# Kernel optimization log

Hardware: AMD Instinct MI355X
Metric: run time of the kernel (lower is better)

The kernel has to match this reference:

```python
import jax, jax.numpy as jnp
import numpy as np

B, N = 8192, 64  # batch of small SPD matrices (SPDnet covariance descriptors)
EPS = 1e-3


def setup_inputs() -> dict:
    key = jax.random.key(0)
    A = jax.random.normal(key, (B, N, N), dtype=jnp.float32)
    # Make strictly SPD: X = A A^T / N + eps*I
    X = jnp.matmul(A, jnp.swapaxes(A, -1, -2)) / N + EPS * jnp.eye(N, dtype=jnp.float32)
    return {"X": X}


def reference(X):
    # LogEig: eigendecompose each SPD matrix, take log of eigenvalues, reconstruct.
    # eigh returns ascending eigenvalues w (b, n) and orthonormal eigenvectors v (b, n, n)
    w, v = jnp.linalg.eigh(X)
    # Y = V diag(log w) V^T
    Y = jnp.einsum('bik,bk,bjk->bij', v, jnp.log(w), v)
    return Y
```

## Files before the change

### kernel.cpp

```cpp
#include <hip/hip_runtime.h>
#include <math.h>

#define NN 4096
#define MAX_SWEEPS 12

typedef float f2 __attribute__((ext_vector_type(2)));

constexpr int psi_step(int k) { return ((k << 1) & 63) ^ ((k & 32) ? 3 : 0); }
struct CycTab {
  int c[63];
  constexpr CycTab() : c{} {
    int x = 1;
    for (int j = 0; j < 63; ++j) { c[j] = x; x = psi_step(x); }
  }
};
static constexpr CycTab CYC{};

__device__ __forceinline__ float bperm(int addr, float x) {
  return __int_as_float(__builtin_amdgcn_ds_bpermute(addr, __float_as_int(x)));
}
__device__ __forceinline__ void wave_lds_fence() {
  asm volatile("s_waitcnt lgkmcnt(0)" ::: "memory");
}

__device__ __forceinline__ f2 colrot(f2 cs, f2 xy) {
  f2 t, d;
  asm("v_pk_mul_f32 %0, %1, %2 op_sel:[1,1] op_sel_hi:[0,1] neg_lo:[1,0]"
      : "=v"(t) : "v"(cs), "v"(xy));
  asm("v_pk_fma_f32 %0, %1, %2, %3 op_sel:[0,0,0] op_sel_hi:[1,0,1]"
      : "=v"(d) : "v"(cs), "v"(xy), "v"(t));
  return d;
}
__device__ __forceinline__ f2 rowrot(f2 cs, f2 a, f2 p) {
  f2 t, d;
  asm("v_pk_mul_f32 %0, %1, %2 op_sel:[1,1] op_sel_hi:[1,0] neg_lo:[1,0] neg_hi:[1,0]"
      : "=v"(t) : "v"(cs), "v"(p));
  asm("v_pk_fma_f32 %0, %1, %2, %3 op_sel:[0,0,0] op_sel_hi:[0,1,1]"
      : "=v"(d) : "v"(cs), "v"(a), "v"(t));
  return d;
}

__global__ __launch_bounds__(256, 2) void logeig_jacobi_pk4(
    const float* __restrict__ X, float* __restrict__ out) {
  __shared__ float SH[4][1024];
  __shared__ f2 ANG[4][64];
  const int tid = threadIdx.x;
  const int lane = tid & 63;
  const int wid = tid >> 6;
  const size_t base = ((size_t)blockIdx.x * 4 + wid) * NN;
  float* lds = SH[wid];
  f2* ang = ANG[wid];

  f2 a2[32], v2[32];

  {
    const float4* Xg = (const float4*)(X + base);
    float4* L4 = (float4*)lds;
    for (int ch = 0; ch < 4; ++ch) {
#pragma unroll
      for (int i = 0; i < 4; ++i) L4[lane + 64 * i] = Xg[ch * 256 + lane + 64 * i];
      wave_lds_fence();
      if ((lane >> 4) == ch) {
        const int lr = (lane & 15) << 6;
#pragma unroll
        for (int r = 0; r < 64; ++r) {
          const float val = lds[lr + (lane ^ r)];
          if (r & 1) a2[r >> 1].y = val; else a2[r >> 1].x = val;
        }
      }
      wave_lds_fence();
    }
  }
#pragma unroll
  for (int t = 1; t < 32; ++t) { v2[t].x = 0.0f; v2[t].y = 0.0f; }
  v2[0].x = 1.0f; v2[0].y = 0.0f;

  int m = 1, B0 = 2, B1 = 4, B2 = 8, B3 = 16, B4 = 32;

#pragma unroll 1
  for (int sw = 0; sw < MAX_SWEEPS; ++sw) {
#pragma unroll 1
    for (int rr = 0; rr < 63; ++rr) {
      const int maddr = (lane ^ m) << 2;
      const float mydg = a2[0].x;
      const float otdg = bperm(maddr, mydg);
      const float apq = 0.5f * (a2[0].y + bperm(maddr, a2[0].y));
      const bool isq = (lane ^ m) < lane;
      const float app = isq ? otdg : mydg;
      const float aqq = isq ? mydg : otdg;
      float c = 1.0f, s = 0.0f;
      if (fabsf(apq) > 1e-37f) {
        const float tau = (aqq - app) / (2.0f * apq);
        float tt = 1.0f / (fabsf(tau) + sqrtf(1.0f + tau * tau));
        tt = (tau >= 0.0f) ? tt : -tt;
        c = rsqrtf(1.0f + tt * tt);
        s = tt * c;
      }
      const float st = isq ? -s : s;
      const f2 cst0 = {c, st};
      ang[lane] = cst0;
      wave_lds_fence();

      {
        const int Bv[5] = {B0, B1, B2, B3, B4};
        int ui = lane;
#pragma unroll
        for (int t = 0; t < 32; ++t) {
          const int slot = t ^ (t >> 1);
          const f2 csg = (t == 0) ? cst0 : ang[ui];
          a2[slot] = colrot(csg, a2[slot]);
          v2[slot] = colrot(csg, v2[slot]);
          if (t < 31) ui ^= Bv[__builtin_ctz(t + 1)];
        }
      }

#pragma unroll
      for (int t = 0; t < 32; ++t) {
        f2 p;
        p.x = bperm(maddr, a2[t].x);
        p.y = bperm(maddr, a2[t].y);
        a2[t] = rowrot(cst0, a2[t], p);
      }

      {
        const int h = CYC.c[0];
        const float ta = (h & 1) ? a2[h >> 1].y : a2[h >> 1].x;
        const float tv = (h & 1) ? v2[h >> 1].y : v2[h >> 1].x;
#pragma unroll
        for (int j = 0; j < 62; ++j) {
          const int dd = CYC.c[j], ss2 = CYC.c[j + 1];
          const float sa = (ss2 & 1) ? a2[ss2 >> 1].y : a2[ss2 >> 1].x;
          const float sv = (ss2 & 1) ? v2[ss2 >> 1].y : v2[ss2 >> 1].x;
          if (dd & 1) { a2[dd >> 1].y = sa; v2[dd >> 1].y = sv; }
          else        { a2[dd >> 1].x = sa; v2[dd >> 1].x = sv; }
        }
        const int l_ = CYC.c[62];
        if (l_ & 1) { a2[l_ >> 1].y = ta; v2[l_ >> 1].y = tv; }
        else        { a2[l_ >> 1].x = ta; v2[l_ >> 1].x = tv; }
      }

      const int nB4 = m ^ B0;
      m = B0; B0 = B1; B1 = B2; B2 = B3; B3 = B4; B4 = nB4;
    }

    float offs = a2[0].y * a2[0].y, dias = a2[0].x * a2[0].x;
#pragma unroll
    for (int t = 1; t < 32; ++t) {
      offs = fmaf(a2[t].x, a2[t].x, offs);
      offs = fmaf(a2[t].y, a2[t].y, offs);
    }
#pragma unroll
    for (int o = 1; o < 64; o <<= 1) {
      offs += __shfl_xor(offs, o);
      dias += __shfl_xor(dias, o);
    }
    if (offs <= 1e-13f * dias) break;
  }

  const float ll = logf(fmaxf(a2[0].x, 1e-30f));
#pragma unroll
  for (int r = 0; r < 64; ++r) {
    const float lr_ = __shfl_xor(ll, r);
    if (r & 1) a2[r >> 1].y = lr_; else a2[r >> 1].x = lr_;
  }
  float* Og = out + base;
  for (int tt = 0; tt < 4; ++tt) {
    if ((lane >> 4) == tt) {
      const int lr = (lane & 15) << 6;
#pragma unroll
      for (int t = 0; t < 32; ++t) {
        const f2 w = v2[t] * a2[t];
        lds[lr + ((2 * t) ^ lane)] = w.x;
        lds[lr + ((2 * t + 1) ^ lane)] = w.y;
      }
    }
    wave_lds_fence();
#pragma unroll 1
    for (int ii = 0; ii < 16; ++ii) {
      const float* Wrow = lds + (ii << 6);
      float acc0 = 0.0f, acc1 = 0.0f;
#pragma unroll
      for (int t = 0; t < 32; ++t) {
        acc0 = fmaf(Wrow[lane ^ (2 * t)], v2[t].x, acc0);
        acc1 = fmaf(Wrow[lane ^ (2 * t + 1)], v2[t].y, acc1);
      }
      Og[((tt << 4) + ii) * 64 + lane] = acc0 + acc1;
    }
    wave_lds_fence();
  }
}

extern "C" void kernel_launch(void* const* d_in, const int* in_sizes, int n_in,
                              void* d_out, int out_size, void* d_ws, size_t ws_size,
                              hipStream_t stream) {
  const float* X = (const float*)d_in[0];
  float* out = (float*)d_out;
  const int nmat = in_sizes[0] / NN;
  logeig_jacobi_pk4<<<nmat / 4, 256, 0, stream>>>(X, out);
}
```

Measured before the change: 5.862 ms.

## Fuse column and row rotations, prefetch next pivot values via bpermute

Fuses the column-rotation and row-rotation loops into one pass. Each slot's partner-lane values are fetched with bpermute before the local column rotation, and the partner's column rotation is recomputed locally with a sign-adjusted variant. It also prefetches the next round's diagonal and off-diagonal partner values early in the loop, taking them off the critical path of the angle computation, and replaces the divisions with hardware reciprocals. This removes one full pass over the registers and overlaps LDS permute latency with arithmetic, at the cost of extra rotation FLOPs and reduced precision in the angle computation.

```diff
diff --git a/kernel.cpp b/kernel.cpp
--- a/kernel.cpp
+++ b/kernel.cpp
@@ -22,12 +22,23 @@
 __device__ __forceinline__ void wave_lds_fence() {
   asm volatile("s_waitcnt lgkmcnt(0)" ::: "memory");
 }
+__device__ __forceinline__ float fast_rcp(float x) {
+  float r; asm("v_rcp_f32 %0, %1" : "=v"(r) : "v"(x)); return r;
+}
 
 __device__ __forceinline__ f2 colrot(f2 cs, f2 xy) {
   f2 t, d;
   asm("v_pk_mul_f32 %0, %1, %2 op_sel:[1,1] op_sel_hi:[0,1] neg_lo:[1,0]"
       : "=v"(t) : "v"(cs), "v"(xy));
   asm("v_pk_fma_f32 %0, %1, %2, %3 op_sel:[0,0,0] op_sel_hi:[1,0,1]"
+      : "=v"(d) : "v"(cs), "v"(xy), "v"(t));
+  return d;
+}
+__device__ __forceinline__ f2 colrotP(f2 cs, f2 xy) {
+  f2 t, d;
+  asm("v_pk_mul_f32 %0, %1, %2 op_sel:[1,1] op_sel_hi:[0,1]"
+      : "=v"(t) : "v"(cs), "v"(xy));
+  asm("v_pk_fma_f32 %0, %1, %2, %3 op_sel:[0,0,0] op_sel_hi:[1,0,1] neg_hi:[1,0,0]"
       : "=v"(d) : "v"(cs), "v"(xy), "v"(t));
   return d;
 }
@@ -77,23 +88,26 @@
 
   int m = 1, B0 = 2, B1 = 4, B2 = 8, B3 = 16, B4 = 32;
 
+  float otdg_pf = bperm((lane ^ 1) << 2, a2[0].x);
+  float sym_pf  = bperm((lane ^ 1) << 2, a2[0].y);
+
 #pragma unroll 1
   for (int sw = 0; sw < MAX_SWEEPS; ++sw) {
 #pragma unroll 1
     for (int rr = 0; rr < 63; ++rr) {
       const int maddr = (lane ^ m) << 2;
       const float mydg = a2[0].x;
-      const float otdg = bperm(maddr, mydg);
-      const float apq = 0.5f * (a2[0].y + bperm(maddr, a2[0].y));
+      const float apq = 0.5f * (a2[0].y + sym_pf);
       const bool isq = (lane ^ m) < lane;
-      const float app = isq ? otdg : mydg;
-      const float aqq = isq ? mydg : otdg;
+      const float app = isq ? otdg_pf : mydg;
+      const float aqq = isq ? mydg : otdg_pf;
       float c = 1.0f, s = 0.0f;
       if (fabsf(apq) > 1e-37f) {
-        const float tau = (aqq - app) / (2.0f * apq);
-        float tt = 1.0f / (fabsf(tau) + sqrtf(1.0f + tau * tau));
+        const float tau = (aqq - app) * 0.5f * fast_rcp(apq);
+        const float den = fabsf(tau) + sqrtf(fmaf(tau, tau, 1.0f));
+        float tt = fast_rcp(den);
         tt = (tau >= 0.0f) ? tt : -tt;
-        c = rsqrtf(1.0f + tt * tt);
+        c = rsqrtf(fmaf(tt, tt, 1.0f));
         s = tt * c;
       }
       const float st = isq ? -s : s;
@@ -107,19 +121,21 @@
 #pragma unroll
         for (int t = 0; t < 32; ++t) {
           const int slot = t ^ (t >> 1);
+          f2 praw;
+          praw.x = bperm(maddr, a2[slot].x);
+          praw.y = bperm(maddr, a2[slot].y);
           const f2 csg = (t == 0) ? cst0 : ang[ui];
-          a2[slot] = colrot(csg, a2[slot]);
+          const f2 tmp = colrot(csg, a2[slot]);
+          const f2 prt = colrotP(csg, praw);
+          a2[slot] = rowrot(cst0, tmp, prt);
           v2[slot] = colrot(csg, v2[slot]);
+          if (t == 1) {
+            const int pmaddr = (lane ^ B0) << 2;
+            otdg_pf = bperm(pmaddr, a2[0].x);
+            sym_pf  = bperm(pmaddr, a2[1].x);
+          }
           if (t < 31) ui ^= Bv[__builtin_ctz(t + 1)];
         }
-      }
-
-#pragma unroll
-      for (int t = 0; t < 32; ++t) {
-        f2 p;
-        p.x = bperm(maddr, a2[t].x);
-        p.y = bperm(maddr, a2[t].y);
-        a2[t] = rowrot(cst0, a2[t], p);
       }
 
       {
```

After: 5.792 ms. About the same (-1.2%).
